# Kernel optimization log

Measured on AMD Instinct MI355X. Metric: run time of the kernel, lower is better.

The kernel has to match this reference:

```python
import jax, jax.numpy as jnp
import numpy as np
from jax import lax


def setup_inputs() -> dict:
    key = jax.random.key(0)
    k1, k2, k3, k4 = jax.random.split(key, 4)
    B, K, Hp, Wp = 512, 64, 5, 5
    num_classes = 10
    x = jax.random.uniform(k1, (B, 1, 20, 20), dtype=jnp.float32)
    patterns = jax.random.uniform(k2, (K, 1, Hp, Wp), dtype=jnp.float32)
    w2 = jax.random.normal(k3, (1, K), dtype=jnp.float32) * 0.1
    b2 = jnp.zeros((1,), dtype=jnp.float32)
    wf = jax.random.normal(k4, (num_classes, 400), dtype=jnp.float32) * 0.05
    bf = jnp.zeros((num_classes,), dtype=jnp.float32)
    return {"x": x, "patterns": patterns, "w2": w2, "b2": b2, "wf": wf, "bf": bf}


def _geneo1(patterns, x):
    # patterns: (K,1,Hp,Wp), x: (B,1,H,W). Same-padded sliding L1 similarity.
    K, _, Hp, Wp = patterns.shape
    P = Hp * Wp
    xp = jnp.pad(x, ((0, 0), (0, 0), (Hp // 2, Hp // 2), (Wp // 2, Wp // 2)))
    # (B, P, H_out, W_out); C=1 so feature order is row-major over (Hp,Wp),
    # matching torch's unfold(2,Hp,1).unfold(3,Wp,1).reshape(-1).
    patches = lax.conv_general_dilated_patches(xp, (Hp, Wp), (1, 1), "VALID")
    pat = patterns.reshape(K, P)
    # (B,K,H_out,W_out): mean_|p| |pattern - patch|
    diff = jnp.abs(pat[None, :, :, None, None] - patches[:, None, :, :, :]).mean(axis=2)
    return 1.0 - diff


def _channel_wise_max(t):
    B, K, H, W = t.shape
    flat = t.reshape(B, K, H * W)
    idx = jnp.argmax(flat, axis=2)                      # (B,K)
    mask = jax.nn.one_hot(idx, H * W, dtype=flat.dtype) # (B,K,HW)
    return (flat * mask).reshape(B, K, H, W)


def reference(x, patterns, w2, b2, wf, bf):
    Fk = _geneo1(patterns, x)            # (B,K,20,20)
    cwm = _channel_wise_max(Fk)          # (B,K,20,20)
    # GENEO2: Linear(K,1) over channel dim (applied on (B,H,W,K))
    t = jnp.einsum("bkhw,ok->bhwo", cwm, w2) + b2   # (B,20,20,1)
    t = jax.nn.sigmoid(t)
    out = t.reshape(t.shape[0], -1) @ wf.T + bf      # (B,num_classes)
    return jax.nn.sigmoid(out)
```

## Files before the change

kernel.cpp:

```cpp
#include <hip/hip_runtime.h>
#include <math.h>

#define NB 512
#define NK 64
#define NP 25
#define HW 400
#define NC 10
#define NWAVE 8

__global__ __launch_bounds__(512, 4) void geneo_mlp_kernel(
    const float* __restrict__ x,
    const float* __restrict__ patterns,
    const float* __restrict__ w2,
    const float* __restrict__ b2,
    const float* __restrict__ wf,
    const float* __restrict__ bf,
    float* __restrict__ out)
{
    __shared__ __align__(16) float xps[4][24 * 24];
    __shared__ __align__(16) float pat_lds[NK * NP];
    __shared__ float  redv[NWAVE][NK];
    __shared__ int    redi[NWAVE][NK];
    __shared__ float2 contrib[NK];
    __shared__ float  wsum[NWAVE][NC];

    const int tid  = threadIdx.x;
    const int b    = blockIdx.x;
    const int lane = tid & 63;
    const int wave = tid >> 6;
    const int rw   = wave >> 2;
    const int cs   = wave & 3;

    #pragma unroll
    for (int cp = 0; cp < 4; ++cp) {
        for (int i = tid; i < 576; i += 512) {
            const int ph = i / 24;
            const int w0 = i - ph * 24;
            const int pc = w0 + cp;
            float v = 0.f;
            if (ph >= 2 && ph < 22 && pc >= 2 && pc < 22)
                v = x[b * HW + (ph - 2) * 20 + (pc - 2)];
            xps[cp][i] = v;
        }
    }
    if (tid < 400)
        reinterpret_cast<float4*>(pat_lds)[tid] =
            reinterpret_cast<const float4*>(patterns)[tid];
    __syncthreads();

    float patv[NP];
    #pragma unroll
    for (int j = 0; j < NP; ++j) patv[j] = pat_lds[lane * NP + j];

    const float* xbase = &xps[cs][cs * 4];
    const int H0   = rw * 10;
    const int col0 = cs * 5;

    float smin = 1e30f;
    int   bi   = 0;
    float Wf[5][9];

    #pragma unroll
    for (int q = 0; q < 5; ++q) {
        const float* rp = xbase + (H0 + q) * 24;
        const float4 a = *reinterpret_cast<const float4*>(rp);
        const float4 c = *reinterpret_cast<const float4*>(rp + 4);
        Wf[q][0] = a.x; Wf[q][1] = a.y; Wf[q][2] = a.z; Wf[q][3] = a.w;
        Wf[q][4] = c.x; Wf[q][5] = c.y; Wf[q][6] = c.z; Wf[q][7] = c.w;
        Wf[q][8] = rp[8];
    }

    #pragma unroll 1
    for (int rr = 0; rr < 2; ++rr) {
        #pragma unroll
        for (int p = 0; p < 5; ++p) {
            const int i = rr * 5 + p;
            const int h = H0 + i;
            #pragma unroll
            for (int px = 0; px < 5; ++px) {
                float s = 0.f;
                #pragma unroll
                for (int dy = 0; dy < 5; ++dy) {
                    const int slot = (p + dy) % 5;
                    #pragma unroll
                    for (int dx = 0; dx < 5; ++dx)
                        s += fabsf(patv[dy * 5 + dx] - Wf[slot][px + dx]);
                }
                const int pix = h * 20 + col0 + px;
                if (s < smin) { smin = s; bi = pix; }
            }
            if (rr * 5 + p < 9) {
                const float* rp = xbase + (h + 5) * 24;
                const float4 a = *reinterpret_cast<const float4*>(rp);
                const float4 c = *reinterpret_cast<const float4*>(rp + 4);
                Wf[p][0] = a.x; Wf[p][1] = a.y; Wf[p][2] = a.z; Wf[p][3] = a.w;
                Wf[p][4] = c.x; Wf[p][5] = c.y; Wf[p][6] = c.z; Wf[p][7] = c.w;
                Wf[p][8] = rp[8];
            }
        }
    }
    redv[wave][lane] = smin;
    redi[wave][lane] = bi;
    __syncthreads();

    if (tid < NK) {
        float v0 = redv[0][tid];
        int   i0 = redi[0][tid];
        #pragma unroll
        for (int w = 1; w < NWAVE; ++w) {
            const float ov = redv[w][tid];
            const int   oi = redi[w][tid];
            if (ov < v0 || (ov == v0 && oi < i0)) { v0 = ov; i0 = oi; }
        }
        const float F = 1.f - v0 * (1.f / 25.f);
        contrib[tid] = make_float2(F * w2[tid], __int_as_float(i0));
    }
    __syncthreads();

    float acc[NC];
    #pragma unroll
    for (int c = 0; c < NC; ++c) acc[c] = 0.f;

    if (tid < HW) {
        float s = b2[0];
        #pragma unroll 8
        for (int k = 0; k < NK; ++k) {
            const float2 cv = contrib[k];
            if (__float_as_int(cv.y) == tid) s += cv.x;
        }
        const float t = 1.f / (1.f + expf(-s));
        #pragma unroll
        for (int c = 0; c < NC; ++c) acc[c] += t * wf[c * HW + tid];
    }

    #pragma unroll
    for (int c = 0; c < NC; ++c) {
        #pragma unroll
        for (int off = 32; off >= 1; off >>= 1)
            acc[c] += __shfl_down(acc[c], off);
    }
    if (lane == 0) {
        #pragma unroll
        for (int c = 0; c < NC; ++c) wsum[wave][c] = acc[c];
    }
    __syncthreads();
    if (tid < NC) {
        float s = bf[tid];
        #pragma unroll
        for (int w = 0; w < NWAVE; ++w) s += wsum[w][tid];
        out[b * NC + tid] = 1.f / (1.f + expf(-s));
    }
}

extern "C" void kernel_launch(void* const* d_in, const int* in_sizes, int n_in,
                              void* d_out, int out_size, void* d_ws, size_t ws_size,
                              hipStream_t stream) {
    const float* x        = (const float*)d_in[0];
    const float* patterns = (const float*)d_in[1];
    const float* w2       = (const float*)d_in[2];
    const float* b2       = (const float*)d_in[3];
    const float* wf       = (const float*)d_in[4];
    const float* bf       = (const float*)d_in[5];
    float* out = (float*)d_out;

    geneo_mlp_kernel<<<NB, 512, 0, stream>>>(x, patterns, w2, b2, wf, bf, out);
}
```

Baseline: 23.80 us.

## Split fused kernel into per-half-image strip kernel plus separate output kernel

The single 512-thread-per-image kernel becomes two kernels. The first launches two 256-thread blocks per image, one per half of the rows, and each loads only its 14-row padded strip. Each block writes its per-channel argmin value and index to workspace. A second kernel merges the two halves and runs the sigmoid/linear/MLP tail. This gives smaller blocks and more of them for better scheduling and occupancy, at the cost of an extra launch, a workspace round trip, and a duplicated pattern load per block.

Result: slower. 24.78 us (+4.1%).

```diff
diff --git a/kernel.cpp b/kernel.cpp
--- a/kernel.cpp
+++ b/kernel.cpp
@@ -6,46 +6,43 @@
 #define NP 25
 #define HW 400
 #define NC 10
-#define NWAVE 8
-
-__global__ __launch_bounds__(512, 4) void geneo_mlp_kernel(
+
+__global__ __launch_bounds__(256, 4) void geneo_strip_kernel(
     const float* __restrict__ x,
     const float* __restrict__ patterns,
-    const float* __restrict__ w2,
-    const float* __restrict__ b2,
-    const float* __restrict__ wf,
-    const float* __restrict__ bf,
-    float* __restrict__ out)
+    float2* __restrict__ ws)
 {
-    __shared__ __align__(16) float xps[4][24 * 24];
+    __shared__ __align__(16) float xps[4][14 * 24];
     __shared__ __align__(16) float pat_lds[NK * NP];
-    __shared__ float  redv[NWAVE][NK];
-    __shared__ int    redi[NWAVE][NK];
-    __shared__ float2 contrib[NK];
-    __shared__ float  wsum[NWAVE][NC];
+    __shared__ float redv[4][NK];
+    __shared__ int   redi[4][NK];
 
     const int tid  = threadIdx.x;
-    const int b    = blockIdx.x;
+    const int blk  = blockIdx.x;
+    const int b    = blk >> 1;
+    const int rw   = blk & 1;
     const int lane = tid & 63;
-    const int wave = tid >> 6;
-    const int rw   = wave >> 2;
-    const int cs   = wave & 3;
+    const int cs   = tid >> 6;
 
     #pragma unroll
     for (int cp = 0; cp < 4; ++cp) {
-        for (int i = tid; i < 576; i += 512) {
-            const int ph = i / 24;
-            const int w0 = i - ph * 24;
+        for (int i = tid; i < 14 * 24; i += 256) {
+            const int lr = i / 24;
+            const int w0 = i - lr * 24;
+            const int pr = rw * 10 + lr;
             const int pc = w0 + cp;
             float v = 0.f;
-            if (ph >= 2 && ph < 22 && pc >= 2 && pc < 22)
-                v = x[b * HW + (ph - 2) * 20 + (pc - 2)];
+            if (pr >= 2 && pr < 22 && pc >= 2 && pc < 22)
+                v = x[b * HW + (pr - 2) * 20 + (pc - 2)];
             xps[cp][i] = v;
         }
     }
-    if (tid < 400)
-        reinterpret_cast<float4*>(pat_lds)[tid] =
-            reinterpret_cast<const float4*>(patterns)[tid];
+    {
+        const float4* p4 = reinterpret_cast<const float4*>(patterns);
+        float4*       l4 = reinterpret_cast<float4*>(pat_lds);
+        l4[tid] = p4[tid];
+        if (tid + 256 < 400) l4[tid + 256] = p4[tid + 256];
+    }
     __syncthreads();
 
     float patv[NP];
@@ -53,7 +50,6 @@
     for (int j = 0; j < NP; ++j) patv[j] = pat_lds[lane * NP + j];
 
     const float* xbase = &xps[cs][cs * 4];
-    const int H0   = rw * 10;
     const int col0 = cs * 5;
 
     float smin = 1e30f;
@@ -62,7 +58,7 @@
 
     #pragma unroll
     for (int q = 0; q < 5; ++q) {
-        const float* rp = xbase + (H0 + q) * 24;
+        const float* rp = xbase + q * 24;
         const float4 a = *reinterpret_cast<const float4*>(rp);
         const float4 c = *reinterpret_cast<const float4*>(rp + 4);
         Wf[q][0] = a.x; Wf[q][1] = a.y; Wf[q][2] = a.z; Wf[q][3] = a.w;
@@ -75,7 +71,6 @@
         #pragma unroll
         for (int p = 0; p < 5; ++p) {
             const int i = rr * 5 + p;
-            const int h = H0 + i;
             #pragma unroll
             for (int px = 0; px < 5; ++px) {
                 float s = 0.f;
@@ -86,11 +81,11 @@
                     for (int dx = 0; dx < 5; ++dx)
                         s += fabsf(patv[dy * 5 + dx] - Wf[slot][px + dx]);
                 }
-                const int pix = h * 20 + col0 + px;
+                const int pix = (rw * 10 + i) * 20 + col0 + px;
                 if (s < smin) { smin = s; bi = pix; }
             }
-            if (rr * 5 + p < 9) {
-                const float* rp = xbase + (h + 5) * 24;
+            if (i < 9) {
+                const float* rp = xbase + (i + 5) * 24;
                 const float4 a = *reinterpret_cast<const float4*>(rp);
                 const float4 c = *reinterpret_cast<const float4*>(rp + 4);
                 Wf[p][0] = a.x; Wf[p][1] = a.y; Wf[p][2] = a.z; Wf[p][3] = a.w;
@@ -99,19 +94,45 @@
             }
         }
     }
-    redv[wave][lane] = smin;
-    redi[wave][lane] = bi;
+    redv[cs][lane] = smin;
+    redi[cs][lane] = bi;
     __syncthreads();
 
     if (tid < NK) {
         float v0 = redv[0][tid];
         int   i0 = redi[0][tid];
         #pragma unroll
-        for (int w = 1; w < NWAVE; ++w) {
+        for (int w = 1; w < 4; ++w) {
             const float ov = redv[w][tid];
             const int   oi = redi[w][tid];
             if (ov < v0 || (ov == v0 && oi < i0)) { v0 = ov; i0 = oi; }
         }
+        ws[blk * NK + tid] = make_float2(v0, __int_as_float(i0));
+    }
+}
+
+__global__ __launch_bounds__(256) void geneo_out_kernel(
+    const float2* __restrict__ ws,
+    const float* __restrict__ w2,
+    const float* __restrict__ b2,
+    const float* __restrict__ wf,
+    const float* __restrict__ bf,
+    float* __restrict__ out)
+{
+    __shared__ float2 contrib[NK];
+    __shared__ float  wsum[4][NC];
+
+    const int tid  = threadIdx.x;
+    const int b    = blockIdx.x;
+    const int lane = tid & 63;
+    const int wave = tid >> 6;
+
+    if (tid < NK) {
+        const float2 c0 = ws[(b * 2 + 0) * NK + tid];
+        const float2 c1 = ws[(b * 2 + 1) * NK + tid];
+        float v0 = c0.x; int i0 = __float_as_int(c0.y);
+        const float v1 = c1.x; const int i1 = __float_as_int(c1.y);
+        if (v1 < v0 || (v1 == v0 && i1 < i0)) { v0 = v1; i0 = i1; }
         const float F = 1.f - v0 * (1.f / 25.f);
         contrib[tid] = make_float2(F * w2[tid], __int_as_float(i0));
     }
@@ -120,17 +141,31 @@
     float acc[NC];
     #pragma unroll
     for (int c = 0; c < NC; ++c) acc[c] = 0.f;
-
-    if (tid < HW) {
-        float s = b2[0];
+    const float b2v = b2[0];
+
+    {
+        const int p0 = tid;
+        float s = b2v;
         #pragma unroll 8
         for (int k = 0; k < NK; ++k) {
             const float2 cv = contrib[k];
-            if (__float_as_int(cv.y) == tid) s += cv.x;
+            if (__float_as_int(cv.y) == p0) s += cv.x;
         }
         const float t = 1.f / (1.f + expf(-s));
         #pragma unroll
-        for (int c = 0; c < NC; ++c) acc[c] += t * wf[c * HW + tid];
+        for (int c = 0; c < NC; ++c) acc[c] += t * wf[c * HW + p0];
+    }
+    if (tid + 256 < HW) {
+        const int p1 = tid + 256;
+        float s = b2v;
+        #pragma unroll 8
+        for (int k = 0; k < NK; ++k) {
+            const float2 cv = contrib[k];
+            if (__float_as_int(cv.y) == p1) s += cv.x;
+        }
+        const float t = 1.f / (1.f + expf(-s));
+        #pragma unroll
+        for (int c = 0; c < NC; ++c) acc[c] += t * wf[c * HW + p1];
     }
 
     #pragma unroll
@@ -145,9 +180,7 @@
     }
     __syncthreads();
     if (tid < NC) {
-        float s = bf[tid];
-        #pragma unroll
-        for (int w = 0; w < NWAVE; ++w) s += wsum[w][tid];
+        const float s = wsum[0][tid] + wsum[1][tid] + wsum[2][tid] + wsum[3][tid] + bf[tid];
         out[b * NC + tid] = 1.f / (1.f + expf(-s));
     }
 }
@@ -162,6 +195,8 @@
     const float* wf       = (const float*)d_in[4];
     const float* bf       = (const float*)d_in[5];
     float* out = (float*)d_out;
-
-    geneo_mlp_kernel<<<NB, 512, 0, stream>>>(x, patterns, w2, b2, wf, bf, out);
+    float2* ws = (float2*)d_ws;
+
+    geneo_strip_kernel<<<NB * 2, 256, 0, stream>>>(x, patterns, ws);
+    geneo_out_kernel<<<NB, 256, 0, stream>>>(ws, w2, b2, wf, bf, out);
 }
```
